# Performance work log

Measured on AMD Instinct MI355X. Metric: run time of the kernel, lower is better.

The kernel has to match this reference:

```python
import jax, jax.numpy as jnp
import numpy as np

D_MODEL = 512
D_INNER = 2 * D_MODEL      # 1024
DT_RANK = D_MODEL // 16    # 32
D_STATE = 16
D_CONV = 4
NB_LAYERS = 3
BATCH = 64
SEQ = 201
CITY = 200
EPS = 1e-5


def setup_inputs() -> dict:
    key = jax.random.key(0)
    ks = jax.random.split(key, 12)
    def rn(k, shape, scale=0.02):
        return jax.random.normal(k, shape, jnp.float32) * scale
    A_init = jnp.tile(jnp.arange(1, D_STATE + 1, dtype=jnp.float32)[None, None, :],
                      (NB_LAYERS, D_INNER, 1))
    return {
        "x": jax.random.uniform(ks[0], (BATCH, SEQ, 2), jnp.float32),
        "city_count": CITY,
        "embed_W": rn(ks[1], (D_MODEL, 2), 0.5),
        "embed_b": jnp.zeros((D_MODEL,), jnp.float32),
        "norm_w": jnp.ones((NB_LAYERS, D_MODEL), jnp.float32),
        "norm_b": jnp.zeros((NB_LAYERS, D_MODEL), jnp.float32),
        "in_W": rn(ks[2], (NB_LAYERS, 2 * D_INNER, D_MODEL)),
        "conv_w": rn(ks[3], (NB_LAYERS, D_INNER, D_CONV), 0.1),
        "conv_b": jnp.zeros((NB_LAYERS, D_INNER), jnp.float32),
        "xproj_W": rn(ks[4], (NB_LAYERS, DT_RANK + 2 * D_STATE, D_INNER)),
        "dtproj_W": rn(ks[5], (NB_LAYERS, D_INNER, DT_RANK), 0.1),
        "dtproj_b": rn(ks[6], (NB_LAYERS, D_INNER), 0.5),
        "A_log": jnp.log(A_init),
        "Dskip": jnp.ones((NB_LAYERS, D_INNER), jnp.float32),
        "out_W": rn(ks[7], (NB_LAYERS, D_MODEL, D_INNER)),
        "normf_w": jnp.ones((D_MODEL,), jnp.float32),
        "normf_b": jnp.zeros((D_MODEL,), jnp.float32),
        "head_W": rn(ks[8], (CITY, D_MODEL)),
    }


def _silu(v):
    return v * jax.nn.sigmoid(v)


def _layernorm(v, w, b):
    v = v.astype(jnp.float32)
    mu = v.mean(-1, keepdims=True)
    var = ((v - mu) ** 2).mean(-1, keepdims=True)
    return (v - mu) * jax.lax.rsqrt(var + EPS) * w + b


def _rmsnorm(v, w, b):
    v = v.astype(jnp.float32)
    ms = (v * v).mean(-1, keepdims=True)
    return v * jax.lax.rsqrt(ms + EPS) * w + b


def _mamba_mixer(h, in_W, cw, cb, xp_W, dt_W, dt_b, A_log, Dv, o_W):
    B, L, _ = h.shape
    xz = jnp.einsum('bld,ed->ble', h, in_W)              # (B,L,2*di)
    xc, z = jnp.split(xz, 2, axis=-1)
    # causal depthwise conv over time
    xt = xc.transpose(0, 2, 1)                           # (B,di,L)
    xt = jax.lax.conv_general_dilated(
        xt, cw[:, None, :], (1,), [(D_CONV - 1, 0)],
        dimension_numbers=('NCH', 'OIH', 'NCH'),
        feature_group_count=D_INNER)
    u = _silu((xt + cb[None, :, None]).transpose(0, 2, 1))   # (B,L,di)
    x_dbl = jnp.einsum('bld,ed->ble', u, xp_W)
    dt_r = x_dbl[..., :DT_RANK]
    Bm = x_dbl[..., DT_RANK:DT_RANK + D_STATE]
    Cm = x_dbl[..., DT_RANK + D_STATE:]
    dt = jax.nn.softplus(jnp.einsum('blr,dr->bld', dt_r, dt_W) + dt_b)
    A = -jnp.exp(A_log)                                  # (di,n)

    def step(hst, ins):
        dt_t, B_t, C_t, u_t = ins                        # (B,di),(B,n),(B,n),(B,di)
        dA = jnp.exp(dt_t[..., None] * A)                # (B,di,n)
        hst = dA * hst + (dt_t * u_t)[..., None] * B_t[:, None, :]
        y = jnp.einsum('bdn,bn->bd', hst, C_t)
        return hst, y

    h0 = jnp.zeros((B, D_INNER, D_STATE), h.dtype)
    _, ys = jax.lax.scan(step, h0, (dt.transpose(1, 0, 2), Bm.transpose(1, 0, 2),
                                    Cm.transpose(1, 0, 2), u.transpose(1, 0, 2)))
    y = ys.transpose(1, 0, 2) + Dv * u
    y = y * _silu(z)
    return jnp.einsum('bld,ed->ble', y, o_W)


def reference(x, city_count, embed_W, embed_b, norm_w, norm_b, in_W, conv_w, conv_b,
              xproj_W, dtproj_W, dtproj_b, A_log, Dskip, out_W, normf_w, normf_b, head_W):
    h = jnp.einsum('blc,dc->bld', x, embed_W) + embed_b
    residual = None
    for i in range(NB_LAYERS):
        residual = h if residual is None else h + residual   # residual in fp32
        hn = _layernorm(residual, norm_w[i], norm_b[i])
        h = _mamba_mixer(hn, in_W[i], conv_w[i], conv_b[i], xproj_W[i],
                         dtproj_W[i], dtproj_b[i], A_log[i], Dskip[i], out_W[i])
    residual = h + residual
    xf = _rmsnorm(residual, normf_w, normf_b)                # final fused RMSNorm
    logits = jnp.einsum('bld,cd->blc', xf, head_W)           # output head -> city logits
    return logits
```

## Files before the change

kernel.cpp:

```cpp
#include <hip/hip_runtime.h>
#include <hip/hip_fp16.h>
#include <math.h>

#define D_MODEL 512
#define D_INNER 1024
#define DT_RANK 32
#define D_STATE 16
#define D_CONV 4
#define NB_LAYERS 3
#define BATCH 64
#define SEQ 201
#define CITY 200
#define M_ROWS (BATCH * SEQ)
#define M_PAD 12928
#define EPS 1e-5f
#define NCH 8
#define CL 26

typedef __attribute__((ext_vector_type(8))) short short8;
typedef __attribute__((ext_vector_type(8))) unsigned short ushort8;
typedef __attribute__((ext_vector_type(4))) float f32x4;

__device__ __forceinline__ float sigmoidf_(float x) { return 1.f / (1.f + __expf(-x)); }

__device__ __forceinline__ unsigned short f2b(float f) {
  union { float f; unsigned int u; } v; v.f = f;
  unsigned int r = (v.u + 0x7fff + ((v.u >> 16) & 1)) >> 16;
  return (unsigned short)r;
}
__device__ __forceinline__ float b2f(unsigned short h) {
  union { unsigned int u; float f; } v; v.u = ((unsigned int)h) << 16; return v.f;
}
__device__ __forceinline__ unsigned short f2h(float f) {
  __half h = __float2half(f); return *(unsigned short*)&h;
}
__device__ __forceinline__ float h2f(unsigned short u) {
  __half h = *(__half*)&u; return __half2float(h);
}

__device__ __forceinline__ void gload_lds16(const void* g, void* l) {
  __builtin_amdgcn_global_load_lds(
      (const __attribute__((address_space(1))) void*)g,
      (__attribute__((address_space(3))) void*)l, 16, 0, 0);
}

__device__ __forceinline__ void exp_vec(float dtv, const float* __restrict__ Areg,
                                        bool fast, float* __restrict__ e) {
  if (fast) {
    float e1 = __expf(-dtv);
    e[0] = e1;
    e[1] = e1 * e1;
    e[2] = e[1] * e1;
    e[3] = e[1] * e[1];
    e[4] = e[3] * e1;
    e[5] = e[3] * e[1];
    e[6] = e[3] * e[2];
    e[7] = e[3] * e[3];
    e[8] = e[7] * e1;
    e[9] = e[7] * e[1];
    e[10] = e[7] * e[2];
    e[11] = e[7] * e[3];
    e[12] = e[7] * e[4];
    e[13] = e[7] * e[5];
    e[14] = e[7] * e[6];
    e[15] = e[7] * e[7];
  } else {
#pragma unroll
    for (int n = 0; n < D_STATE; ++n) e[n] = __expf(dtv * Areg[n]);
  }
}
__device__ __forceinline__ bool a_is_arange(const float* __restrict__ Areg) {
  bool f = true;
#pragma unroll
  for (int n = 0; n < D_STATE; ++n)
    f = f && (fabsf(Areg[n] + (float)(n + 1)) < 1e-4f * (float)(n + 1));
  return f;
}

__global__ __launch_bounds__(256) void k_f2b(const float* __restrict__ in,
                                             unsigned short* __restrict__ out,
                                             int n, int n_total) {
  int i = blockIdx.x * 256 + threadIdx.x;
  if (i < n) out[i] = f2b(in[i]);
  else if (i < n_total) out[i] = 0;
}

__global__ __launch_bounds__(256) void k_padR(const float* __restrict__ W,
                                              unsigned short* __restrict__ out,
                                              int nl, int inrows, int outrows, int cols) {
  int i = blockIdx.x * 256 + threadIdx.x;
  if (i >= nl * outrows * cols) return;
  int c = i % cols;
  int r = (i / cols) % outrows;
  int L = i / (cols * outrows);
  out[i] = (r < inrows) ? f2b(W[((size_t)L * inrows + r) * cols + c]) : 0;
}

__global__ __launch_bounds__(256) void k_convT(const float* __restrict__ cw,
                                               float* __restrict__ cwT) {
  int i = blockIdx.x * 256 + threadIdx.x;
  if (i >= NB_LAYERS * D_CONV * D_INNER) return;
  int d = i & (D_INNER - 1);
  int k = (i >> 10) & 3;
  int L = i >> 12;
  cwT[i] = cw[((size_t)L * D_INNER + d) * D_CONV + k];
}

__global__ __launch_bounds__(256) void k_embed(const float* __restrict__ x,
                                               const float* __restrict__ W,
                                               const float* __restrict__ b,
                                               float* __restrict__ res) {
  int idx = blockIdx.x * 256 + threadIdx.x;
  if (idx >= M_ROWS * D_MODEL) return;
  int d = idx & (D_MODEL - 1);
  int m = idx >> 9;
  float x0 = x[m * 2 + 0], x1 = x[m * 2 + 1];
  res[idx] = fmaf(x0, W[d * 2 + 0], fmaf(x1, W[d * 2 + 1], b[d]));
}

__global__ __launch_bounds__(256) void k_norm(const float* __restrict__ res,
                                              unsigned short* __restrict__ out_b,
                                              const float* __restrict__ w,
                                              const float* __restrict__ b,
                                              int mode) {
  int row = blockIdx.x * 4 + (threadIdx.x >> 6);
  int lane = threadIdx.x & 63;
  if (row >= M_ROWS) return;
  const float* rp = res + (size_t)row * D_MODEL;
  float v[8];
#pragma unroll
  for (int j = 0; j < 8; ++j) v[j] = rp[j * 64 + lane];
  float mu = 0.f, rstd;
  if (mode == 0) {
    float s = 0.f;
#pragma unroll
    for (int j = 0; j < 8; ++j) s += v[j];
#pragma unroll
    for (int o = 1; o < 64; o <<= 1) s += __shfl_xor(s, o);
    mu = s * (1.f / D_MODEL);
    float vs = 0.f;
#pragma unroll
    for (int j = 0; j < 8; ++j) { float d0 = v[j] - mu; vs += d0 * d0; }
#pragma unroll
    for (int o = 1; o < 64; o <<= 1) vs += __shfl_xor(vs, o);
    rstd = rsqrtf(vs * (1.f / D_MODEL) + EPS);
  } else {
    float s = 0.f;
#pragma unroll
    for (int j = 0; j < 8; ++j) s += v[j] * v[j];
#pragma unroll
    for (int o = 1; o < 64; o <<= 1) s += __shfl_xor(s, o);
    rstd = rsqrtf(s * (1.f / D_MODEL) + EPS);
  }
#pragma unroll
  for (int j = 0; j < 8; ++j) {
    int c = j * 64 + lane;
    out_b[(size_t)row * D_MODEL + c] = f2b((v[j] - mu) * rstd * w[c] + b[c]);
  }
}

template <int BOUT, int ADDRES>
__global__ __launch_bounds__(256) void k_gemm_mfma(const unsigned short* __restrict__ A,
                                                   const unsigned short* __restrict__ B,
                                                   void* __restrict__ Cv, int ldc,
                                                   int M, int Nout, int K) {
  __shared__ unsigned short lA[2][128 * 64];
  __shared__ unsigned short lB[2][128 * 64];
  int tid = threadIdx.x;
  int wave = tid >> 6, lane = tid & 63;
  int nx = gridDim.x;
  int nwg = nx * gridDim.y;
  int bid = blockIdx.y * nx + blockIdx.x;
  int q = nwg >> 3, rr = nwg & 7;
  int xcd = bid & 7, idx = bid >> 3;
  int swz = (xcd < rr ? xcd * (q + 1) : rr * (q + 1) + (xcd - rr) * q) + idx;
  int bm = (swz / nx) * 128, bn = (swz % nx) * 128;
  int wm = (wave >> 1) * 64, wn = (wave & 1) * 64;
  f32x4 acc[4][4] = {};

  auto stage = [&](int kt, int bb) {
    int k0 = kt * 64;
#pragma unroll
    for (int i = 0; i < 4; ++i) {
      int e = (i * 256 + tid) * 8;
      int r = e >> 6, c = e & 63;
      int csrc = c ^ ((r & 7) << 3);
      gload_lds16(A + (size_t)(bm + r) * K + k0 + csrc, &lA[bb][e]);
      gload_lds16(B + (size_t)(bn + r) * K + k0 + csrc, &lB[bb][e]);
    }
  };

  int nk = K >> 6;
  stage(0, 0);
  __syncthreads();
  for (int t = 0; t < nk; ++t) {
    int cur = t & 1;
    if (t + 1 < nk) stage(t + 1, cur ^ 1);
#pragma unroll
    for (int ks = 0; ks < 2; ++ks) {
      int koff = ks * 32 + (lane >> 4) * 8;
      short8 a[4], b[4];
#pragma unroll
      for (int i = 0; i < 4; ++i) {
        int row = wm + i * 16 + (lane & 15);
        a[i] = *(const short8*)&lA[cur][row * 64 + (koff ^ ((row & 7) << 3))];
      }
#pragma unroll
      for (int j = 0; j < 4; ++j) {
        int row = wn + j * 16 + (lane & 15);
        b[j] = *(const short8*)&lB[cur][row * 64 + (koff ^ ((row & 7) << 3))];
      }
#pragma unroll
      for (int i = 0; i < 4; ++i)
#pragma unroll
        for (int j = 0; j < 4; ++j)
          acc[i][j] = __builtin_amdgcn_mfma_f32_16x16x32_bf16(a[i], b[j], acc[i][j], 0, 0, 0);
    }
    __syncthreads();
  }
#pragma unroll
  for (int i = 0; i < 4; ++i) {
    int row0 = bm + wm + i * 16 + (lane >> 4) * 4;
#pragma unroll
    for (int j = 0; j < 4; ++j) {
      int col = bn + wn + j * 16 + (lane & 15);
#pragma unroll
      for (int r = 0; r < 4; ++r) {
        int m = row0 + r;
        if (m < M && col < Nout) {
          float v = acc[i][j][r];
          if (ADDRES) {
            float* cp = (float*)Cv + (size_t)m * ldc + col;
            *cp = *cp + v;
          } else if (BOUT == 1) {
            ((unsigned short*)Cv)[(size_t)m * ldc + col] = f2b(v);
          } else {
            ((float*)Cv)[(size_t)m * ldc + col] = v;
          }
        }
      }
    }
  }
}

__global__ __launch_bounds__(256) void k_conv_silu(const unsigned short* __restrict__ xz,
                                                   const float* __restrict__ cwT,
                                                   const float* __restrict__ cb,
                                                   unsigned short* __restrict__ ub) {
  int i = blockIdx.x * 256 + threadIdx.x;
  if (i >= M_ROWS * 128) return;
  int dg = (i & 127) << 3;
  int m = i >> 7;
  int l = m % SEQ;
  float y[8];
  float4 cb0 = *(const float4*)&cb[dg];
  float4 cb1 = *(const float4*)&cb[dg + 4];
  y[0] = cb0.x; y[1] = cb0.y; y[2] = cb0.z; y[3] = cb0.w;
  y[4] = cb1.x; y[5] = cb1.y; y[6] = cb1.z; y[7] = cb1.w;
#pragma unroll
  for (int k = 0; k < D_CONV; ++k) {
    int ls = l - (D_CONV - 1) + k;
    if (ls >= 0) {
      ushort8 xv = *(const ushort8*)&xz[(size_t)(m - (D_CONV - 1) + k) * 2048 + dg];
      float4 w0 = *(const float4*)&cwT[k * D_INNER + dg];
      float4 w1 = *(const float4*)&cwT[k * D_INNER + dg + 4];
      y[0] = fmaf(w0.x, b2f(xv[0]), y[0]);
      y[1] = fmaf(w0.y, b2f(xv[1]), y[1]);
      y[2] = fmaf(w0.z, b2f(xv[2]), y[2]);
      y[3] = fmaf(w0.w, b2f(xv[3]), y[3]);
      y[4] = fmaf(w1.x, b2f(xv[4]), y[4]);
      y[5] = fmaf(w1.y, b2f(xv[5]), y[5]);
      y[6] = fmaf(w1.z, b2f(xv[6]), y[6]);
      y[7] = fmaf(w1.w, b2f(xv[7]), y[7]);
    }
  }
  ushort8 o;
#pragma unroll
  for (int j = 0; j < 8; ++j) { float v = y[j]; v = v * sigmoidf_(v); o[j] = f2b(v); }
  *(ushort8*)&ub[(size_t)m * D_INNER + dg] = o;
}

__device__ __forceinline__ float dt_eval(const float* __restrict__ xq,
                                         const float* __restrict__ Wd, float bias) {
  float a0 = 0.f, a1 = 0.f, a2 = 0.f, a3 = 0.f;
#pragma unroll
  for (int r = 0; r < 2; ++r) {
    float4 q0 = *(const float4*)&xq[r * 16 + 0];
    float4 q1 = *(const float4*)&xq[r * 16 + 4];
    float4 q2 = *(const float4*)&xq[r * 16 + 8];
    float4 q3 = *(const float4*)&xq[r * 16 + 12];
    int o = r * 16;
    a0 = fmaf(q0.x, Wd[o + 0], a0); a0 = fmaf(q0.y, Wd[o + 1], a0);
    a0 = fmaf(q0.z, Wd[o + 2], a0); a0 = fmaf(q0.w, Wd[o + 3], a0);
    a1 = fmaf(q1.x, Wd[o + 4], a1); a1 = fmaf(q1.y, Wd[o + 5], a1);
    a1 = fmaf(q1.z, Wd[o + 6], a1); a1 = fmaf(q1.w, Wd[o + 7], a1);
    a2 = fmaf(q2.x, Wd[o + 8], a2); a2 = fmaf(q2.y, Wd[o + 9], a2);
    a2 = fmaf(q2.z, Wd[o + 10], a2); a2 = fmaf(q2.w, Wd[o + 11], a2);
    a3 = fmaf(q3.x, Wd[o + 12], a3); a3 = fmaf(q3.y, Wd[o + 13], a3);
    a3 = fmaf(q3.z, Wd[o + 14], a3); a3 = fmaf(q3.w, Wd[o + 15], a3);
  }
  float dot = ((a0 + a1) + (a2 + a3)) + bias;
  return (dot > 20.f) ? dot : __logf(1.f + __expf(dot));
}

__global__ __launch_bounds__(256) void k_scan_p1(const unsigned short* __restrict__ ub,
                                                 const float* __restrict__ xdb,
                                                 const float* __restrict__ dtW,
                                                 const float* __restrict__ dtb,
                                                 const float* __restrict__ A_log,
                                                 unsigned short* __restrict__ dt,
                                                 unsigned short* __restrict__ L,
                                                 float* __restrict__ dtsum) {
  int tid = threadIdx.x;
  int b = blockIdx.x >> 3, c = blockIdx.x & 7;
  int d = blockIdx.y * 256 + tid;
  int t0 = c * CL, t1 = t0 + CL < SEQ ? t0 + CL : SEQ;
  float Wd[DT_RANK];
#pragma unroll
  for (int r = 0; r < DT_RANK; r += 4) {
    float4 w4 = *(const float4*)&dtW[(size_t)d * DT_RANK + r];
    Wd[r] = w4.x; Wd[r + 1] = w4.y; Wd[r + 2] = w4.z; Wd[r + 3] = w4.w;
  }
  float bias = dtb[d];
  float Areg[D_STATE], hst[D_STATE];
#pragma unroll
  for (int n = 0; n < D_STATE; ++n) {
    Areg[n] = -__expf(A_log[d * D_STATE + n]);
    hst[n] = 0.f;
  }
  bool fast = a_is_arange(Areg);
  float ds = 0.f;
  size_t row0 = (size_t)b * SEQ;
  for (int t = t0; t < t1; ++t) {
    size_t m = row0 + t;
    const float* xq = xdb + m * 64;
    unsigned short dh = f2h(dt_eval(xq, Wd, bias));
    dt[m * D_INNER + d] = dh;
    float dtv = h2f(dh);
    float uv = b2f(ub[m * D_INNER + d]);
    float Bv[D_STATE];
#pragma unroll
    for (int qd = 0; qd < 4; ++qd) {
      float4 v4 = *(const float4*)&xq[32 + qd * 4];
      Bv[qd * 4 + 0] = v4.x; Bv[qd * 4 + 1] = v4.y;
      Bv[qd * 4 + 2] = v4.z; Bv[qd * 4 + 3] = v4.w;
    }
    float du = dtv * uv;
    ds += dtv;
    float e[D_STATE];
    exp_vec(dtv, Areg, fast, e);
#pragma unroll
    for (int j = 0; j < D_STATE; ++j)
      hst[j] = fmaf(e[j], hst[j], du * Bv[j]);
  }
  size_t base = ((size_t)(b * NCH + c) * D_INNER + d) * D_STATE;
  ushort8 o0, o1;
#pragma unroll
  for (int j = 0; j < 8; ++j) { o0[j] = f2b(hst[j]); o1[j] = f2b(hst[8 + j]); }
  *(ushort8*)&L[base] = o0;
  *(ushort8*)&L[base + 8] = o1;
  dtsum[(size_t)(b * NCH + c) * D_INNER + d] = ds;
}

__global__ __launch_bounds__(256) void k_scan_fix(const float* __restrict__ A_log,
                                                  const float* __restrict__ dtsum,
                                                  unsigned short* __restrict__ L) {
  int tid = threadIdx.x;
  int b = blockIdx.x;
  int d = blockIdx.y * 256 + tid;
  float Areg[D_STATE], h[D_STATE];
#pragma unroll
  for (int n = 0; n < D_STATE; ++n) {
    Areg[n] = -__expf(A_log[d * D_STATE + n]);
    h[n] = 0.f;
  }
  bool fast = a_is_arange(Areg);
  for (int c = 0; c < NCH; ++c) {
    size_t base = ((size_t)(b * NCH + c) * D_INNER + d) * D_STATE;
    ushort8 l0 = *(const ushort8*)&L[base];
    ushort8 l1 = *(const ushort8*)&L[base + 8];
    float ds = dtsum[(size_t)(b * NCH + c) * D_INNER + d];
    ushort8 o0, o1;
#pragma unroll
    for (int j = 0; j < 8; ++j) { o0[j] = f2b(h[j]); o1[j] = f2b(h[8 + j]); }
    *(ushort8*)&L[base] = o0;
    *(ushort8*)&L[base + 8] = o1;
    float e[D_STATE];
    exp_vec(ds, Areg, fast, e);
#pragma unroll
    for (int j = 0; j < 8; ++j)
      h[j] = fmaf(e[j], h[j], b2f(l0[j]));
#pragma unroll
    for (int j = 0; j < 8; ++j)
      h[8 + j] = fmaf(e[8 + j], h[8 + j], b2f(l1[j]));
  }
}

__global__ __launch_bounds__(256) void k_scan_p2(const unsigned short* __restrict__ xz,
                                                 const unsigned short* __restrict__ ub,
                                                 const float* __restrict__ xdb,
                                                 const unsigned short* __restrict__ dt,
                                                 const float* __restrict__ A_log,
                                                 const float* __restrict__ Dv,
                                                 const unsigned short* __restrict__ L,
                                                 unsigned short* __restrict__ yb) {
  int tid = threadIdx.x;
  int b = blockIdx.x >> 3, c = blockIdx.x & 7;
  int d = blockIdx.y * 256 + tid;
  int t0 = c * CL, t1 = t0 + CL < SEQ ? t0 + CL : SEQ;
  float Areg[D_STATE], hst[D_STATE];
  size_t base = ((size_t)(b * NCH + c) * D_INNER + d) * D_STATE;
  ushort8 l0 = *(const ushort8*)&L[base];
  ushort8 l1 = *(const ushort8*)&L[base + 8];
#pragma unroll
  for (int n = 0; n < D_STATE; ++n) Areg[n] = -__expf(A_log[d * D_STATE + n]);
  bool fast = a_is_arange(Areg);
#pragma unroll
  for (int j = 0; j < 8; ++j) { hst[j] = b2f(l0[j]); hst[8 + j] = b2f(l1[j]); }
  float Dd = Dv[d];
  size_t row0 = (size_t)b * SEQ;
  for (int t = t0; t < t1; ++t) {
    size_t m = row0 + t;
    const float* xq = xdb + m * 64;
    float dtv = h2f(dt[m * D_INNER + d]);
    float uv = b2f(ub[m * D_INNER + d]);
    float zv = b2f(xz[m * 2048 + 1024 + d]);
    float Bv[D_STATE], Cvv[D_STATE];
#pragma unroll
    for (int qd = 0; qd < 4; ++qd) {
      float4 v4 = *(const float4*)&xq[32 + qd * 4];
      Bv[qd * 4 + 0] = v4.x; Bv[qd * 4 + 1] = v4.y;
      Bv[qd * 4 + 2] = v4.z; Bv[qd * 4 + 3] = v4.w;
      float4 c4 = *(const float4*)&xq[48 + qd * 4];
      Cvv[qd * 4 + 0] = c4.x; Cvv[qd * 4 + 1] = c4.y;
      Cvv[qd * 4 + 2] = c4.z; Cvv[qd * 4 + 3] = c4.w;
    }
    float du = dtv * uv;
    float e[D_STATE];
    exp_vec(dtv, Areg, fast, e);
    float y0 = 0.f, y1 = 0.f, y2 = 0.f, y3 = 0.f;
#pragma unroll
    for (int j = 0; j < D_STATE; ++j) {
      hst[j] = fmaf(e[j], hst[j], du * Bv[j]);
      float& yq = (j < 4) ? y0 : (j < 8) ? y1 : (j < 12) ? y2 : y3;
      yq = fmaf(hst[j], Cvv[j], yq);
    }
    float y = (y0 + y1) + (y2 + y3);
    y = fmaf(Dd, uv, y);
    y = y * (zv * sigmoidf_(zv));
    yb[m * D_INNER + d] = f2b(y);
  }
}

extern "C" void kernel_launch(void* const* d_in, const int* in_sizes, int n_in,
                              void* d_out, int out_size, void* d_ws, size_t ws_size,
                              hipStream_t stream) {
  const float* x        = (const float*)d_in[0];
  const float* embed_W  = (const float*)d_in[2];
  const float* embed_b  = (const float*)d_in[3];
  const float* norm_w   = (const float*)d_in[4];
  const float* norm_b   = (const float*)d_in[5];
  const float* in_W     = (const float*)d_in[6];
  const float* conv_w   = (const float*)d_in[7];
  const float* conv_b   = (const float*)d_in[8];
  const float* xproj_W  = (const float*)d_in[9];
  const float* dtproj_W = (const float*)d_in[10];
  const float* dtproj_b = (const float*)d_in[11];
  const float* A_log    = (const float*)d_in[12];
  const float* Dskip    = (const float*)d_in[13];
  const float* out_W    = (const float*)d_in[14];
  const float* normf_w  = (const float*)d_in[15];
  const float* normf_b  = (const float*)d_in[16];
  const float* head_W   = (const float*)d_in[17];
  float* out = (float*)d_out;

  size_t f32_elems = (size_t)M_ROWS * 512  + (size_t)M_PAD * 64  +
                     (size_t)NB_LAYERS * D_CONV * D_INNER  +
                     (size_t)BATCH * NCH * D_INNER ;
  size_t bf16_elems = (size_t)M_ROWS * 2048  + (size_t)M_PAD * 2048  +
                      (size_t)M_ROWS * 1024  +
                      (size_t)BATCH * NCH * D_INNER * D_STATE  +
                      (size_t)NB_LAYERS * (2048 * 512 + 512 * 1024 + 128 * 1024) +
                      256 * 512;
  size_t need = f32_elems * 4 + bf16_elems * 2;
  if (ws_size < need) return;

  float* ws = (float*)d_ws;
  float* buf_res  = ws;
  float* buf_xdb  = buf_res  + (size_t)M_ROWS * 512;
  float* buf_cwT  = buf_xdb  + (size_t)M_PAD * 64;
  float* buf_dts  = buf_cwT  + (size_t)NB_LAYERS * D_CONV * D_INNER;
  unsigned short* buf_xz   = (unsigned short*)(buf_dts + (size_t)BATCH * NCH * D_INNER);
  unsigned short* buf_ub   = buf_xz + (size_t)M_ROWS * 2048;
  unsigned short* buf_yb   = buf_ub + (size_t)M_PAD * 1024;
  unsigned short* buf_hnb  = buf_yb;
  unsigned short* buf_dt   = buf_yb + (size_t)M_PAD * 1024;
  unsigned short* buf_L    = buf_dt + (size_t)M_ROWS * 1024;
  unsigned short* buf_wib  = buf_L + (size_t)BATCH * NCH * D_INNER * D_STATE;
  unsigned short* buf_wob  = buf_wib + (size_t)NB_LAYERS * 2048 * 512;
  unsigned short* buf_wxb  = buf_wob + (size_t)NB_LAYERS * 512 * 1024;
  unsigned short* buf_whb  = buf_wxb + (size_t)NB_LAYERS * 128 * 1024;

  dim3 blk(256);

  k_f2b<<<(NB_LAYERS * 2048 * 512 + 255) / 256, blk, 0, stream>>>(
      in_W, buf_wib, NB_LAYERS * 2048 * 512, NB_LAYERS * 2048 * 512);
  k_f2b<<<(NB_LAYERS * 512 * 1024 + 255) / 256, blk, 0, stream>>>(
      out_W, buf_wob, NB_LAYERS * 512 * 1024, NB_LAYERS * 512 * 1024);
  k_padR<<<(NB_LAYERS * 128 * 1024 + 255) / 256, blk, 0, stream>>>(
      xproj_W, buf_wxb, NB_LAYERS, 64, 128, 1024);
  k_f2b<<<(256 * 512 + 255) / 256, blk, 0, stream>>>(head_W, buf_whb, CITY * 512, 256 * 512);
  k_convT<<<(NB_LAYERS * D_CONV * D_INNER + 255) / 256, blk, 0, stream>>>(conv_w, buf_cwT);

  k_embed<<<(M_ROWS * D_MODEL + 255) / 256, blk, 0, stream>>>(x, embed_W, embed_b, buf_res);

  for (int i = 0; i < NB_LAYERS; ++i) {
    k_norm<<<(M_ROWS + 3) / 4, blk, 0, stream>>>(
        buf_res, buf_hnb, norm_w + i * D_MODEL, norm_b + i * D_MODEL, 0);

    k_gemm_mfma<1, 0><<<dim3(2048 / 128, M_PAD / 128), blk, 0, stream>>>(
        buf_hnb, buf_wib + (size_t)i * 2048 * 512, buf_xz, 2048, M_ROWS, 2048, 512);

    k_conv_silu<<<(M_ROWS * 128 + 255) / 256, blk, 0, stream>>>(
        buf_xz, buf_cwT + (size_t)i * D_CONV * D_INNER, conv_b + (size_t)i * D_INNER, buf_ub);

    k_gemm_mfma<0, 0><<<dim3(1, M_PAD / 128), blk, 0, stream>>>(
        buf_ub, buf_wxb + (size_t)i * 128 * 1024, buf_xdb, 64, M_ROWS, 64, 1024);

    const float* Ai  = A_log + (size_t)i * D_INNER * D_STATE;
    const float* Wdt = dtproj_W + (size_t)i * D_INNER * DT_RANK;
    const float* bdt = dtproj_b + (size_t)i * D_INNER;
    k_scan_p1<<<dim3(BATCH * NCH, D_INNER / 256), blk, 0, stream>>>(
        buf_ub, buf_xdb, Wdt, bdt, Ai, buf_dt, buf_L, buf_dts);
    k_scan_fix<<<dim3(BATCH, D_INNER / 256), blk, 0, stream>>>(Ai, buf_dts, buf_L);
    k_scan_p2<<<dim3(BATCH * NCH, D_INNER / 256), blk, 0, stream>>>(
        buf_xz, buf_ub, buf_xdb, buf_dt, Ai, Dskip + (size_t)i * D_INNER, buf_L, buf_yb);

    k_gemm_mfma<0, 1><<<dim3(512 / 128, M_PAD / 128), blk, 0, stream>>>(
        buf_yb, buf_wob + (size_t)i * 512 * 1024, buf_res, 512, M_ROWS, 512, 1024);
  }

  k_norm<<<(M_ROWS + 3) / 4, blk, 0, stream>>>(buf_res, buf_hnb, normf_w, normf_b, 1);

  k_gemm_mfma<0, 0><<<dim3(256 / 128, M_PAD / 128), blk, 0, stream>>>(
      buf_hnb, buf_whb, out, CITY, M_ROWS, CITY, 512);
}
```

Before: 746.6 us.

## Single-buffer GEMM LDS tiles and fuse SiLU(z) into in-proj epilogue

The MFMA GEMM drops its double-buffered LDS prefetch in favour of a single shared tile with load-sync-compute-sync per K step. This halves shared memory per block, which may allow more resident blocks per CU, but it gives up the overlap of global loads with MFMA work. Separately, the input projection GEMM now applies SiLU to the z half in its epilogue, so the scan kernel only multiplies by the stored gate instead of computing a sigmoid per element. Because the gate is now rounded to bf16 after SiLU rather than before, results shift slightly.

```diff
diff --git a/kernel.cpp b/kernel.cpp
--- a/kernel.cpp
+++ b/kernel.cpp
@@ -159,13 +159,13 @@
   }
 }
 
-template <int BOUT, int ADDRES>
+template <int BOUT, int ADDRES, int ZGATE>
 __global__ __launch_bounds__(256) void k_gemm_mfma(const unsigned short* __restrict__ A,
                                                    const unsigned short* __restrict__ B,
                                                    void* __restrict__ Cv, int ldc,
                                                    int M, int Nout, int K) {
-  __shared__ unsigned short lA[2][128 * 64];
-  __shared__ unsigned short lB[2][128 * 64];
+  __shared__ unsigned short lA[128 * 64];
+  __shared__ unsigned short lB[128 * 64];
   int tid = threadIdx.x;
   int wave = tid >> 6, lane = tid & 63;
   int nx = gridDim.x;
@@ -178,24 +178,16 @@
   int wm = (wave >> 1) * 64, wn = (wave & 1) * 64;
   f32x4 acc[4][4] = {};
 
-  auto stage = [&](int kt, int bb) {
-    int k0 = kt * 64;
+  for (int k0 = 0; k0 < K; k0 += 64) {
 #pragma unroll
     for (int i = 0; i < 4; ++i) {
       int e = (i * 256 + tid) * 8;
       int r = e >> 6, c = e & 63;
       int csrc = c ^ ((r & 7) << 3);
-      gload_lds16(A + (size_t)(bm + r) * K + k0 + csrc, &lA[bb][e]);
-      gload_lds16(B + (size_t)(bn + r) * K + k0 + csrc, &lB[bb][e]);
-    }
-  };
-
-  int nk = K >> 6;
-  stage(0, 0);
-  __syncthreads();
-  for (int t = 0; t < nk; ++t) {
-    int cur = t & 1;
-    if (t + 1 < nk) stage(t + 1, cur ^ 1);
+      gload_lds16(A + (size_t)(bm + r) * K + k0 + csrc, &lA[e]);
+      gload_lds16(B + (size_t)(bn + r) * K + k0 + csrc, &lB[e]);
+    }
+    __syncthreads();
 #pragma unroll
     for (int ks = 0; ks < 2; ++ks) {
       int koff = ks * 32 + (lane >> 4) * 8;
@@ -203,12 +195,12 @@
 #pragma unroll
       for (int i = 0; i < 4; ++i) {
         int row = wm + i * 16 + (lane & 15);
-        a[i] = *(const short8*)&lA[cur][row * 64 + (koff ^ ((row & 7) << 3))];
+        a[i] = *(const short8*)&lA[row * 64 + (koff ^ ((row & 7) << 3))];
       }
 #pragma unroll
       for (int j = 0; j < 4; ++j) {
         int row = wn + j * 16 + (lane & 15);
-        b[j] = *(const short8*)&lB[cur][row * 64 + (koff ^ ((row & 7) << 3))];
+        b[j] = *(const short8*)&lB[row * 64 + (koff ^ ((row & 7) << 3))];
       }
 #pragma unroll
       for (int i = 0; i < 4; ++i)
@@ -233,6 +225,7 @@
             float* cp = (float*)Cv + (size_t)m * ldc + col;
             *cp = *cp + v;
           } else if (BOUT == 1) {
+            if (ZGATE && col >= 1024) v = v * sigmoidf_(v);
             ((unsigned short*)Cv)[(size_t)m * ldc + col] = f2b(v);
           } else {
             ((float*)Cv)[(size_t)m * ldc + col] = v;
@@ -424,7 +417,7 @@
     const float* xq = xdb + m * 64;
     float dtv = h2f(dt[m * D_INNER + d]);
     float uv = b2f(ub[m * D_INNER + d]);
-    float zv = b2f(xz[m * 2048 + 1024 + d]);
+    float zg = b2f(xz[m * 2048 + 1024 + d]);
     float Bv[D_STATE], Cvv[D_STATE];
 #pragma unroll
     for (int qd = 0; qd < 4; ++qd) {
@@ -447,7 +440,7 @@
     }
     float y = (y0 + y1) + (y2 + y3);
     y = fmaf(Dd, uv, y);
-    y = y * (zv * sigmoidf_(zv));
+    y = y * zg;
     yb[m * D_INNER + d] = f2b(y);
   }
 }
@@ -518,13 +511,13 @@
     k_norm<<<(M_ROWS + 3) / 4, blk, 0, stream>>>(
         buf_res, buf_hnb, norm_w + i * D_MODEL, norm_b + i * D_MODEL, 0);
 
-    k_gemm_mfma<1, 0><<<dim3(2048 / 128, M_PAD / 128), blk, 0, stream>>>(
+    k_gemm_mfma<1, 0, 1><<<dim3(2048 / 128, M_PAD / 128), blk, 0, stream>>>(
         buf_hnb, buf_wib + (size_t)i * 2048 * 512, buf_xz, 2048, M_ROWS, 2048, 512);
 
     k_conv_silu<<<(M_ROWS * 128 + 255) / 256, blk, 0, stream>>>(
         buf_xz, buf_cwT + (size_t)i * D_CONV * D_INNER, conv_b + (size_t)i * D_INNER, buf_ub);
 
-    k_gemm_mfma<0, 0><<<dim3(1, M_PAD / 128), blk, 0, stream>>>(
+    k_gemm_mfma<0, 0, 0><<<dim3(1, M_PAD / 128), blk, 0, stream>>>(
         buf_ub, buf_wxb + (size_t)i * 128 * 1024, buf_xdb, 64, M_ROWS, 64, 1024);
 
     const float* Ai  = A_log + (size_t)i * D_INNER * D_STATE;
@@ -536,12 +529,12 @@
     k_scan_p2<<<dim3(BATCH * NCH, D_INNER / 256), blk, 0, stream>>>(
         buf_xz, buf_ub, buf_xdb, buf_dt, Ai, Dskip + (size_t)i * D_INNER, buf_L, buf_yb);
 
-    k_gemm_mfma<0, 1><<<dim3(512 / 128, M_PAD / 128), blk, 0, stream>>>(
+    k_gemm_mfma<0, 1, 0><<<dim3(512 / 128, M_PAD / 128), blk, 0, stream>>>(
         buf_yb, buf_wob + (size_t)i * 512 * 1024, buf_res, 512, M_ROWS, 512, 1024);
   }
 
   k_norm<<<(M_ROWS + 3) / 4, blk, 0, stream>>>(buf_res, buf_hnb, normf_w, normf_b, 1);
 
-  k_gemm_mfma<0, 0><<<dim3(256 / 128, M_PAD / 128), blk, 0, stream>>>(
+  k_gemm_mfma<0, 0, 0><<<dim3(256 / 128, M_PAD / 128), blk, 0, stream>>>(
       buf_hnb, buf_whb, out, CITY, M_ROWS, CITY, 512);
 }
```

Result: slower. 782.5 us (+4.8%).
